# Kernel optimization log

Hardware: AMD Instinct MI355X
Metric: run time of the kernel (lower is better)

## Reference

```python
import jax, jax.numpy as jnp
import numpy as np

N = 1024        # nodes; B == N required by the source's broadcasting
C2 = 64         # 2 * in_channels (x feature dim)
E = 64          # embed_dim
ALPHA = 0.2     # leaky relu negative slope
NEG = -1e12     # mask fill value from source


def setup_inputs() -> dict:
    key = jax.random.key(0)
    k1, k2, k3, k4, k5 = jax.random.split(key, 5)
    x = jax.random.normal(k1, (N, N, C2), dtype=jnp.float32)
    adj = (jax.random.uniform(k2, (N, N)) > 0.9).astype(jnp.float32)
    gain = 1.414
    W = jax.random.uniform(k3, (C2, E), jnp.float32, -1.0, 1.0) * (gain * np.sqrt(6.0 / (C2 + E)))
    a = jax.random.uniform(k4, (E, 1), jnp.float32, -1.0, 1.0) * (gain * np.sqrt(6.0 / (E + 1)))
    b = jax.random.normal(k5, (E,), dtype=jnp.float32) * 0.02
    return {"x": x, "adj": adj, "W": W, "a": a, "b": b}


def reference(x, adj, W, a, b):
    # x: [B, N, 2C] with B == N; W: [2C, E]
    wx = jnp.einsum('bnc,ce->bne', x, W)                    # [B, N, E]
    # per-node scalar attention logit, squeeze(-1) -> [B, N]
    s = jnp.squeeze(jax.nn.leaky_relu(wx, ALPHA) @ a, -1)   # [B, N]
    # adjacency masking: [B,N] + [N,N] broadcasts to [N,N] since B == N
    scores = s + jnp.where(adj > 0.0, 0.0, NEG)             # [N, N]
    att = jax.nn.softmax(scores, axis=-1)                   # [N, N]
    # 2-D attention broadcast over batch: out[b] = att @ wx[b]
    out = jnp.einsum('ij,bje->bie', att, wx) + b            # [B, N, E]
    return out
```

## Files before the change

kernel.cpp:

```cpp
#include <hip/hip_runtime.h>
#include <stdint.h>

#define N_NODES 1024
#define C2v 64
#define EMB 64
#define ALPHA 0.2f
#define NEG_FILL (-1e12f)

typedef __attribute__((ext_vector_type(8))) short short8v;
typedef __attribute__((ext_vector_type(4))) float float4v;
typedef unsigned int u32;

static __device__ __forceinline__ short f2bf(float f) {
    unsigned u = __builtin_bit_cast(unsigned, f);
    u = (u + 0x7FFFu + ((u >> 16) & 1u)) >> 16;
    return (short)(unsigned short)u;
}
static __device__ __forceinline__ u32 pack2bf(float a, float b) {
    return (u32)(unsigned short)f2bf(a) | ((u32)(unsigned short)f2bf(b) << 16);
}
static __device__ __forceinline__ void gload16(const float* g, float* l) {
    __builtin_amdgcn_global_load_lds(
        (const __attribute__((address_space(1))) u32*)g,
        (__attribute__((address_space(3))) u32*)l, 16, 0, 0);
}

__global__ __launch_bounds__(256) void k_wx(const float* __restrict__ x,
                                            const float* __restrict__ adj,
                                            const float* __restrict__ W,
                                            const float* __restrict__ a,
                                            unsigned short* __restrict__ wxT,
                                            unsigned short* __restrict__ att) {
    __shared__ float xs[2][4096];
    __shared__ float s_lds[N_NODES];
    __shared__ float red[8];

    const int i   = blockIdx.x;
    const int tid = threadIdx.x;
    const int w   = tid >> 6;
    const int l   = tid & 63;
    const int g   = l >> 4;
    const int m   = l & 15;

    short8v wfrag[4][2];
#pragma unroll
    for (int nt = 0; nt < 4; ++nt)
#pragma unroll
        for (int ks = 0; ks < 2; ++ks) {
            short8v v;
#pragma unroll
            for (int ii = 0; ii < 8; ++ii)
                v[ii] = f2bf(W[(ks * 32 + g * 8 + ii) * EMB + nt * 16 + m]);
            wfrag[nt][ks] = v;
        }
    float afrag[4];
#pragma unroll
    for (int nt = 0; nt < 4; ++nt) afrag[nt] = a[nt * 16 + m];

    const float* xi = x + (size_t)i * N_NODES * C2v;

    auto STAGE = [&](int jt, int buf) {
#pragma unroll
        for (int q = 0; q < 4; ++q) {
            const int row  = w * 16 + q * 4 + g;
            const int slot = m ^ (row & 7);
            gload16(xi + (size_t)(jt * 64 + row) * C2v + slot * 4,
                    &xs[buf][w * 1024 + q * 256]);
        }
    };

    STAGE(0, 0);
#pragma unroll
    for (int jt = 0; jt < 16; ++jt) {
        const int buf = jt & 1;
        if (jt < 15) STAGE(jt + 1, buf ^ 1);
        if (jt < 15) { asm volatile("s_waitcnt vmcnt(4)" ::: "memory"); }
        else         { asm volatile("s_waitcnt vmcnt(0)" ::: "memory"); }
        __builtin_amdgcn_sched_barrier(0);

        const int j0 = jt * 64 + w * 16;
        float4v acc[4];
#pragma unroll
        for (int nt = 0; nt < 4; ++nt) acc[nt] = (float4v)0.0f;

#pragma unroll
        for (int ks = 0; ks < 2; ++ks) {
            const int slo = (ks * 8 + 2 * g) ^ (m & 7);
            const int shi = (ks * 8 + 2 * g + 1) ^ (m & 7);
            const float4v lo = *(const float4v*)&xs[buf][w * 1024 + m * 64 + slo * 4];
            const float4v hi = *(const float4v*)&xs[buf][w * 1024 + m * 64 + shi * 4];
            short8v afr;
            afr[0] = f2bf(lo[0]); afr[1] = f2bf(lo[1]);
            afr[2] = f2bf(lo[2]); afr[3] = f2bf(lo[3]);
            afr[4] = f2bf(hi[0]); afr[5] = f2bf(hi[1]);
            afr[6] = f2bf(hi[2]); afr[7] = f2bf(hi[3]);
#pragma unroll
            for (int nt = 0; nt < 4; ++nt)
                acc[nt] = __builtin_amdgcn_mfma_f32_16x16x32_bf16(
                    afr, wfrag[nt][ks], acc[nt], 0, 0, 0);
        }

#pragma unroll
        for (int nt = 0; nt < 4; ++nt) {
            uint2 pk;
            pk.x = pack2bf(acc[nt][0], acc[nt][1]);
            pk.y = pack2bf(acc[nt][2], acc[nt][3]);
            *(uint2*)&wxT[((size_t)i * EMB + nt * 16 + m) * N_NODES + j0 + g * 4] = pk;
        }

#pragma unroll
        for (int r = 0; r < 4; ++r) {
            float v = 0.f;
#pragma unroll
            for (int nt = 0; nt < 4; ++nt) {
                float t = acc[nt][r];
                t = (t > 0.f) ? t : (ALPHA * t);
                v += t * afrag[nt];
            }
            v += __shfl_xor(v, 1);
            v += __shfl_xor(v, 2);
            v += __shfl_xor(v, 4);
            v += __shfl_xor(v, 8);
            if (m == 0) s_lds[j0 + g * 4 + r] = v;
        }
    }
    __syncthreads();

    const float* adjrow = adj + (size_t)i * N_NODES;
    float sc[4];
    float lmax = -3.4e38f;
#pragma unroll
    for (int q = 0; q < 4; ++q) {
        int j = tid + q * 256;
        float v = s_lds[j] + (adjrow[j] > 0.f ? 0.f : NEG_FILL);
        sc[q] = v;
        lmax = fmaxf(lmax, v);
    }
#pragma unroll
    for (int d = 1; d < 64; d <<= 1) lmax = fmaxf(lmax, __shfl_xor(lmax, d));
    if (l == 0) red[w] = lmax;
    __syncthreads();
    const float M = fmaxf(fmaxf(red[0], red[1]), fmaxf(red[2], red[3]));

    float ex[4];
    float lsum = 0.f;
#pragma unroll
    for (int q = 0; q < 4; ++q) {
        ex[q] = __expf(sc[q] - M);
        lsum += ex[q];
    }
#pragma unroll
    for (int d = 1; d < 64; d <<= 1) lsum += __shfl_xor(lsum, d);
    __syncthreads();
    if (l == 0) red[w] = lsum;
    __syncthreads();
    const float S = red[0] + red[1] + red[2] + red[3];
    const float inv = 1.0f / S;

    unsigned short* arow = att + (size_t)i * N_NODES;
#pragma unroll
    for (int q = 0; q < 4; ++q) {
        int j = tid + q * 256;
        arow[j] = (unsigned short)f2bf(ex[q] * inv);
    }
}

__global__ __launch_bounds__(256) void k_out2(const unsigned short* __restrict__ wxT,
                                              const unsigned short* __restrict__ att,
                                              const float* __restrict__ bias,
                                              float* __restrict__ out) {
    const int hw = blockIdx.x;
    const int L  = (hw & 7) * 512 + (hw >> 3);
    const int b  = L >> 2;
    const int it = L & 3;

    const int tid = threadIdx.x;
    const int w   = tid >> 6;
    const int l   = tid & 63;
    const int g   = l >> 4;
    const int m   = l & 15;

    const int i0 = it * 256 + w * 64;
    const size_t abase = (size_t)(i0 + m) * N_NODES;
    const size_t bbase = ((size_t)b * EMB + m) * N_NODES;

    float4v acc[4][4];
#pragma unroll
    for (int mt = 0; mt < 4; ++mt)
#pragma unroll
        for (int nt = 0; nt < 4; ++nt) acc[mt][nt] = (float4v)0.0f;

    for (int kt = 0; kt < 16; ++kt) {
#pragma unroll
        for (int ks = 0; ks < 2; ++ks) {
            const int jc = kt * 64 + ks * 32 + g * 8;
            short8v afr[4], bfr[4];
#pragma unroll
            for (int mt = 0; mt < 4; ++mt)
                afr[mt] = *(const short8v*)&att[abase + (size_t)mt * 16 * N_NODES + jc];
#pragma unroll
            for (int nt = 0; nt < 4; ++nt)
                bfr[nt] = *(const short8v*)&wxT[bbase + (size_t)nt * 16 * N_NODES + jc];
#pragma unroll
            for (int mt = 0; mt < 4; ++mt)
#pragma unroll
                for (int nt = 0; nt < 4; ++nt)
                    acc[mt][nt] = __builtin_amdgcn_mfma_f32_16x16x32_bf16(
                        afr[mt], bfr[nt], acc[mt][nt], 0, 0, 0);
        }
    }

    float bv[4];
#pragma unroll
    for (int nt = 0; nt < 4; ++nt) bv[nt] = bias[nt * 16 + m];

#pragma unroll
    for (int mt = 0; mt < 4; ++mt)
#pragma unroll
        for (int nt = 0; nt < 4; ++nt)
#pragma unroll
            for (int r = 0; r < 4; ++r) {
                const int i = i0 + mt * 16 + g * 4 + r;
                out[((size_t)b * N_NODES + i) * EMB + nt * 16 + m] = acc[mt][nt][r] + bv[nt];
            }
}

__global__ __launch_bounds__(256) void k_att_fb(const float* __restrict__ x,
                                                const float* __restrict__ adj,
                                                const float* __restrict__ W,
                                                const float* __restrict__ a,
                                                unsigned short* __restrict__ att) {
    __shared__ float s_lds[N_NODES];
    __shared__ float red[8];
    const int i = blockIdx.x, tid = threadIdx.x;
    const int w = tid >> 6, l = tid & 63, g = l >> 4, m = l & 15;
    short8v wfrag[4][2];
#pragma unroll
    for (int nt = 0; nt < 4; ++nt)
#pragma unroll
        for (int ks = 0; ks < 2; ++ks) {
            short8v v;
#pragma unroll
            for (int ii = 0; ii < 8; ++ii)
                v[ii] = f2bf(W[(ks * 32 + g * 8 + ii) * EMB + nt * 16 + m]);
            wfrag[nt][ks] = v;
        }
    float afrag[4];
#pragma unroll
    for (int nt = 0; nt < 4; ++nt) afrag[nt] = a[nt * 16 + m];
    const float* xi = x + (size_t)i * N_NODES * C2v;
    for (int jt = 0; jt < N_NODES / 64; ++jt) {
        const int j0 = jt * 64 + w * 16;
        float4v acc[4];
#pragma unroll
        for (int nt = 0; nt < 4; ++nt) acc[nt] = (float4v)0.0f;
#pragma unroll
        for (int ks = 0; ks < 2; ++ks) {
            const float* p = xi + (size_t)(j0 + m) * C2v + ks * 32 + g * 8;
            float4v lo = *(const float4v*)p;
            float4v hi = *(const float4v*)(p + 4);
            short8v afr;
            afr[0] = f2bf(lo[0]); afr[1] = f2bf(lo[1]);
            afr[2] = f2bf(lo[2]); afr[3] = f2bf(lo[3]);
            afr[4] = f2bf(hi[0]); afr[5] = f2bf(hi[1]);
            afr[6] = f2bf(hi[2]); afr[7] = f2bf(hi[3]);
#pragma unroll
            for (int nt = 0; nt < 4; ++nt)
                acc[nt] = __builtin_amdgcn_mfma_f32_16x16x32_bf16(afr, wfrag[nt][ks], acc[nt], 0, 0, 0);
        }
#pragma unroll
        for (int r = 0; r < 4; ++r) {
            float v = 0.f;
#pragma unroll
            for (int nt = 0; nt < 4; ++nt) {
                float t = acc[nt][r];
                t = (t > 0.f) ? t : (ALPHA * t);
                v += t * afrag[nt];
            }
            v += __shfl_xor(v, 1); v += __shfl_xor(v, 2);
            v += __shfl_xor(v, 4); v += __shfl_xor(v, 8);
            if (m == 0) s_lds[j0 + g * 4 + r] = v;
        }
    }
    __syncthreads();
    const float* adjrow = adj + (size_t)i * N_NODES;
    float sc[4]; float lmax = -3.4e38f;
#pragma unroll
    for (int q = 0; q < 4; ++q) {
        int j = tid + q * 256;
        float v = s_lds[j] + (adjrow[j] > 0.f ? 0.f : NEG_FILL);
        sc[q] = v; lmax = fmaxf(lmax, v);
    }
#pragma unroll
    for (int d = 1; d < 64; d <<= 1) lmax = fmaxf(lmax, __shfl_xor(lmax, d));
    if (l == 0) red[w] = lmax;
    __syncthreads();
    const float M = fmaxf(fmaxf(red[0], red[1]), fmaxf(red[2], red[3]));
    float ex[4]; float lsum = 0.f;
#pragma unroll
    for (int q = 0; q < 4; ++q) { ex[q] = __expf(sc[q] - M); lsum += ex[q]; }
#pragma unroll
    for (int d = 1; d < 64; d <<= 1) lsum += __shfl_xor(lsum, d);
    __syncthreads();
    if (l == 0) red[w] = lsum;
    __syncthreads();
    const float S = red[0] + red[1] + red[2] + red[3];
    const float inv = 1.0f / S;
    unsigned short* arow = att + (size_t)i * N_NODES;
#pragma unroll
    for (int q = 0; q < 4; ++q) {
        int j = tid + q * 256;
        arow[j] = (unsigned short)f2bf(ex[q] * inv);
    }
}

__global__ __launch_bounds__(256) void k_out_fb(const float* __restrict__ x,
                                                const unsigned short* __restrict__ att,
                                                const float* __restrict__ W,
                                                const float* __restrict__ bias,
                                                float* __restrict__ out) {
    __shared__ __attribute__((aligned(16))) short tmp_lds[256][72];
    const int hw = blockIdx.x;
    const int L  = (hw & 7) * 512 + (hw >> 3);
    const int b  = L >> 2;
    const int it = L & 3;
    const int tid = threadIdx.x;
    const int w = tid >> 6, l = tid & 63, g = l >> 4, m = l & 15;
    float4v acc[4][4];
#pragma unroll
    for (int mt = 0; mt < 4; ++mt)
#pragma unroll
        for (int nt = 0; nt < 4; ++nt) acc[mt][nt] = (float4v)0.0f;
    const float* xb = x + (size_t)b * N_NODES * C2v;
    for (int kt = 0; kt < 16; ++kt) {
        const int j0 = kt * 64;
        short8v afr[4][2];
#pragma unroll
    for (int mt = 0; mt < 4; ++mt)
#pragma unroll
            for (int ks = 0; ks < 2; ++ks) {
                const int row = it * 256 + w * 64 + mt * 16 + m;
                afr[mt][ks] = *(const short8v*)&att[(size_t)row * N_NODES + j0 + ks * 32 + g * 8];
            }
        short8v bfr[4][2];
#pragma unroll
        for (int nt = 0; nt < 4; ++nt)
#pragma unroll
            for (int ks = 0; ks < 2; ++ks) {
                short8v v;
#pragma unroll
                for (int ii = 0; ii < 8; ++ii) {
                    const int j = j0 + ks * 32 + g * 8 + ii;
                    v[ii] = f2bf(xb[(size_t)j * C2v + nt * 16 + m]);
                }
                bfr[nt][ks] = v;
            }
#pragma unroll
        for (int mt = 0; mt < 4; ++mt)
#pragma unroll
            for (int nt = 0; nt < 4; ++nt)
#pragma unroll
                for (int ks = 0; ks < 2; ++ks)
                    acc[mt][nt] = __builtin_amdgcn_mfma_f32_16x16x32_bf16(
                        afr[mt][ks], bfr[nt][ks], acc[mt][nt], 0, 0, 0);
    }
#pragma unroll
    for (int mt = 0; mt < 4; ++mt)
#pragma unroll
        for (int nt = 0; nt < 4; ++nt)
#pragma unroll
            for (int r = 0; r < 4; ++r)
                tmp_lds[w * 64 + mt * 16 + g * 4 + r][nt * 16 + m] = f2bf(acc[mt][nt][r]);
    __syncthreads();
    short8v wfrag[4][2];
#pragma unroll
    for (int nt = 0; nt < 4; ++nt)
#pragma unroll
        for (int ks = 0; ks < 2; ++ks) {
            short8v v;
#pragma unroll
            for (int ii = 0; ii < 8; ++ii)
                v[ii] = f2bf(W[(ks * 32 + g * 8 + ii) * EMB + nt * 16 + m]);
            wfrag[nt][ks] = v;
        }
    float bfrag[4];
#pragma unroll
    for (int nt = 0; nt < 4; ++nt) bfrag[nt] = bias[nt * 16 + m];
    float4v acc2[4][4];
#pragma unroll
    for (int mt = 0; mt < 4; ++mt)
#pragma unroll
        for (int nt = 0; nt < 4; ++nt) acc2[mt][nt] = (float4v)0.0f;
#pragma unroll
    for (int mt = 0; mt < 4; ++mt)
#pragma unroll
        for (int ks = 0; ks < 2; ++ks) {
            const short8v a2 = *(const short8v*)&tmp_lds[w * 64 + mt * 16 + m][ks * 32 + g * 8];
#pragma unroll
            for (int nt = 0; nt < 4; ++nt)
                acc2[mt][nt] = __builtin_amdgcn_mfma_f32_16x16x32_bf16(a2, wfrag[nt][ks], acc2[mt][nt], 0, 0, 0);
        }
#pragma unroll
    for (int mt = 0; mt < 4; ++mt)
#pragma unroll
        for (int nt = 0; nt < 4; ++nt)
#pragma unroll
            for (int r = 0; r < 4; ++r) {
                const int i = it * 256 + w * 64 + mt * 16 + g * 4 + r;
                out[((size_t)b * N_NODES + i) * EMB + nt * 16 + m] = acc2[mt][nt][r] + bfrag[nt];
            }
}

extern "C" void kernel_launch(void* const* d_in, const int* in_sizes, int n_in,
                              void* d_out, int out_size, void* d_ws, size_t ws_size,
                              hipStream_t stream) {
    const float* x    = (const float*)d_in[0];
    const float* adj  = (const float*)d_in[1];
    const float* W    = (const float*)d_in[2];
    const float* a    = (const float*)d_in[3];
    const float* bias = (const float*)d_in[4];
    float* out = (float*)d_out;

    const size_t WXT_BYTES = (size_t)N_NODES * EMB * N_NODES * 2;
    const size_t ATT_BYTES = (size_t)N_NODES * N_NODES * 2;

    if (ws_size >= WXT_BYTES + ATT_BYTES) {
        unsigned short* wxT = (unsigned short*)d_ws;
        unsigned short* att = (unsigned short*)((char*)d_ws + WXT_BYTES);
        k_wx<<<N_NODES, 256, 0, stream>>>(x, adj, W, a, wxT, att);
        k_out2<<<4096, 256, 0, stream>>>(wxT, att, bias, out);
    } else {
        unsigned short* att = (unsigned short*)d_ws;
        k_att_fb<<<N_NODES, 256, 0, stream>>>(x, adj, W, a, att);
        k_out_fb<<<4096, 256, 0, stream>>>(x, att, W, bias, out);
    }
}
```

Measured before the change: 933.2 us.

## Double-buffer wxT tiles through LDS and prefetch attention fragments in k_out2

k_out2 now stages each 64x64 wxT tile into swizzled LDS with async global_load_lds, double-buffered per wave. Attention fragments for the next k-step are prefetched into registers while the current step's MFMAs run, and wave priority is raised around the MFMA block. The k_wx pipeline's waitcnt is loosened to vmcnt(8) for middle iterations. The aim is to hide global load latency in the output GEMM, at the cost of more registers and LDS; the looser waitcnt in k_wx may risk reading a buffer before its load has finished.

```diff
diff --git a/kernel.cpp b/kernel.cpp
--- a/kernel.cpp
+++ b/kernel.cpp
@@ -19,7 +19,7 @@
 static __device__ __forceinline__ u32 pack2bf(float a, float b) {
     return (u32)(unsigned short)f2bf(a) | ((u32)(unsigned short)f2bf(b) << 16);
 }
-static __device__ __forceinline__ void gload16(const float* g, float* l) {
+static __device__ __forceinline__ void gload16v(const void* g, void* l) {
     __builtin_amdgcn_global_load_lds(
         (const __attribute__((address_space(1))) u32*)g,
         (__attribute__((address_space(3))) u32*)l, 16, 0, 0);
@@ -64,8 +64,8 @@
         for (int q = 0; q < 4; ++q) {
             const int row  = w * 16 + q * 4 + g;
             const int slot = m ^ (row & 7);
-            gload16(xi + (size_t)(jt * 64 + row) * C2v + slot * 4,
-                    &xs[buf][w * 1024 + q * 256]);
+            gload16v(xi + (size_t)(jt * 64 + row) * C2v + slot * 4,
+                     &xs[buf][w * 1024 + q * 256]);
         }
     };
 
@@ -74,8 +74,9 @@
     for (int jt = 0; jt < 16; ++jt) {
         const int buf = jt & 1;
         if (jt < 15) STAGE(jt + 1, buf ^ 1);
-        if (jt < 15) { asm volatile("s_waitcnt vmcnt(4)" ::: "memory"); }
-        else         { asm volatile("s_waitcnt vmcnt(0)" ::: "memory"); }
+        if (jt == 0)      { asm volatile("s_waitcnt vmcnt(4)" ::: "memory"); }
+        else if (jt < 15) { asm volatile("s_waitcnt vmcnt(8)" ::: "memory"); }
+        else              { asm volatile("s_waitcnt vmcnt(0)" ::: "memory"); }
         __builtin_amdgcn_sched_barrier(0);
 
         const int j0 = jt * 64 + w * 16;
@@ -169,6 +170,8 @@
                                               const unsigned short* __restrict__ att,
                                               const float* __restrict__ bias,
                                               float* __restrict__ out) {
+    __shared__ short wlds[2][4][4096];
+
     const int hw = blockIdx.x;
     const int L  = (hw & 7) * 512 + (hw >> 3);
     const int b  = L >> 2;
@@ -182,7 +185,26 @@
 
     const int i0 = it * 256 + w * 64;
     const size_t abase = (size_t)(i0 + m) * N_NODES;
-    const size_t bbase = ((size_t)b * EMB + m) * N_NODES;
+    const unsigned short* wxb = wxT + (size_t)b * EMB * N_NODES;
+
+    auto STAGE = [&](int kt, int buf) {
+#pragma unroll
+        for (int p = 0; p < 8; ++p) {
+            const int e  = p * 8 + (l >> 3);
+            const int sd = l & 7;
+            const int ss = sd ^ (e & 7);
+            gload16v(wxb + (size_t)e * N_NODES + kt * 64 + ss * 8,
+                     &wlds[buf][w][p * 512]);
+        }
+    };
+    auto ATTLOAD = [&](short8v dst[4][2], int kt) {
+#pragma unroll
+        for (int mt = 0; mt < 4; ++mt)
+#pragma unroll
+            for (int ks = 0; ks < 2; ++ks)
+                dst[mt][ks] = *(const short8v*)&att[abase + (size_t)mt * 16 * N_NODES
+                                                   + kt * 64 + ks * 32 + g * 8];
+    };
 
     float4v acc[4][4];
 #pragma unroll
@@ -190,23 +212,46 @@
 #pragma unroll
         for (int nt = 0; nt < 4; ++nt) acc[mt][nt] = (float4v)0.0f;
 
+    short8v cur[4][2], nxt[4][2];
+    STAGE(0, 0);
+    ATTLOAD(cur, 0);
+
+#pragma unroll
     for (int kt = 0; kt < 16; ++kt) {
-#pragma unroll
-        for (int ks = 0; ks < 2; ++ks) {
-            const int jc = kt * 64 + ks * 32 + g * 8;
-            short8v afr[4], bfr[4];
-#pragma unroll
-            for (int mt = 0; mt < 4; ++mt)
-                afr[mt] = *(const short8v*)&att[abase + (size_t)mt * 16 * N_NODES + jc];
-#pragma unroll
-            for (int nt = 0; nt < 4; ++nt)
-                bfr[nt] = *(const short8v*)&wxT[bbase + (size_t)nt * 16 * N_NODES + jc];
+        const int buf = kt & 1;
+        if (kt < 15) {
+            STAGE(kt + 1, buf ^ 1);
+            ATTLOAD(nxt, kt + 1);
+            asm volatile("s_waitcnt vmcnt(16)" ::: "memory");
+        } else {
+            asm volatile("s_waitcnt vmcnt(0)" ::: "memory");
+        }
+        __builtin_amdgcn_sched_barrier(0);
+
+        const char* base = (const char*)&wlds[buf][w][0];
+        __builtin_amdgcn_s_setprio(1);
+#pragma unroll
+        for (int ks = 0; ks < 2; ++ks) {
+            short8v bfr[4];
+#pragma unroll
+            for (int nt = 0; nt < 4; ++nt) {
+                const int e = nt * 16 + m;
+                bfr[nt] = *(const short8v*)(base + e * 128 + (((ks * 4 + g) ^ (m & 7)) << 4));
+            }
 #pragma unroll
             for (int mt = 0; mt < 4; ++mt)
 #pragma unroll
                 for (int nt = 0; nt < 4; ++nt)
                     acc[mt][nt] = __builtin_amdgcn_mfma_f32_16x16x32_bf16(
-                        afr[mt], bfr[nt], acc[mt][nt], 0, 0, 0);
+                        cur[mt][ks], bfr[nt], acc[mt][nt], 0, 0, 0);
+        }
+        __builtin_amdgcn_s_setprio(0);
+
+        if (kt < 15) {
+#pragma unroll
+            for (int mt = 0; mt < 4; ++mt)
+#pragma unroll
+                for (int ks = 0; ks < 2; ++ks) cur[mt][ks] = nxt[mt][ks];
         }
     }
 
@@ -336,7 +381,7 @@
         const int j0 = kt * 64;
         short8v afr[4][2];
 #pragma unroll
-    for (int mt = 0; mt < 4; ++mt)
+        for (int mt = 0; mt < 4; ++mt)
 #pragma unroll
             for (int ks = 0; ks < 2; ++ks) {
                 const int row = it * 256 + w * 64 + mt * 16 + m;
```

Measured after the change: 769.2 us. -17.6%, faster.
